# Kernel optimization log

Measured on AMD Instinct MI355X. Metric: run time of the kernel, lower is better.

The kernel has to match this reference:

```python
import jax, jax.numpy as jnp
import numpy as np

WINDOW_SIZE = 5
CONSISTENCY_WEIGHT = 1.0


def _wsum(x, w):
    # sliding-window sum along axis 1 via exclusive cumsum differences
    s = jnp.cumsum(x, axis=1)
    s = jnp.pad(s, ((0, 0), (1, 0)))
    return s[:, w:] - s[:, :-w]  # [B, L-w+1]


def setup_inputs() -> dict:
    key = jax.random.key(0)
    k1, k2, k3 = jax.random.split(key, 3)
    B, L, C = 512, 16384, 2
    return {
        "predictions": jax.random.normal(k1, (B, L, C), dtype=jnp.float32),
        "targets": jax.random.randint(k2, (B, L), 0, 2, dtype=jnp.int32),
        "mask": jax.random.randint(k3, (B, L), 0, 2, dtype=jnp.int32),
    }


def reference(predictions, targets, mask):
    w = WINDOW_SIZE
    probs = jax.nn.softmax(predictions, axis=-1)[..., 1]  # [B, L]
    t = targets.astype(jnp.float32)
    m = mask.astype(jnp.float32)

    msum = _wsum(m, w)                       # [B, W]
    denom = jnp.maximum(msum, 1.0)           # clamp(min=1.0)
    spm = _wsum(probs * m, w)
    stm = _wsum(t * m, w)
    sp2m = _wsum(probs * probs * m, w)
    st2m = _wsum(t * t * m, w)

    pmean = spm / denom
    tmean = stm / denom
    # masked biased variance: sum((x - mean)^2 * m) / clamp(msum, 1)
    pvar = (sp2m - 2.0 * pmean * spm + pmean * pmean * msum) / denom
    tvar = (st2m - 2.0 * tmean * stm + tmean * tmean * msum) / denom

    mse = jnp.mean((pvar - tvar) ** 2, axis=0)          # per-window MSE over batch, [W]
    valid = (jnp.sum(msum, axis=0) > 0).astype(jnp.float32)  # skip windows with zero mask
    cnt = jnp.maximum(jnp.sum(valid), 1.0)
    loss = jnp.sum(mse * valid) / cnt * CONSISTENCY_WEIGHT
    return loss
```

## Files before the change

### kernel.cpp

```cpp
#include <hip/hip_runtime.h>
#include <math.h>

#define BATCH 512
#define LEN   16384
#define WIN   5
#define WOUT  (LEN - WIN + 1)
#define TPB   256
#define TILE  256
#define ELEMS (TILE + WIN - 1)

__global__ void bcl_partial_kernel(const float* __restrict__ pred,
                                   const int*   __restrict__ tgt,
                                   const int*   __restrict__ msk,
                                   float* __restrict__ part_d2,
                                   float* __restrict__ part_ms,
                                   int bper) {
    __shared__ float s_m[ELEMS], s_tm[ELEMS], s_pm[ELEMS], s_p2m[ELEMS];

    const int tile0 = blockIdx.x * TILE;
    const int j     = tile0 + threadIdx.x;
    const int b0    = blockIdx.y * bper;

    float accd2 = 0.f, accms = 0.f;

    for (int b = b0; b < b0 + bper; ++b) {
        __syncthreads();
        for (int i = threadIdx.x; i < ELEMS; i += TPB) {
            const int e = tile0 + i;
            float m = 0.f, tmf = 0.f, p = 0.f;
            if (e < LEN) {
                const size_t base = (size_t)b * LEN + e;
                const int    mi = msk[base];
                const int    ti = tgt[base];
                const float2 p2 = ((const float2*)pred)[base];
                p   = 1.0f / (1.0f + __expf(p2.x - p2.y));
                m   = (float)mi;
                tmf = (float)(ti & mi);
            }
            s_m[i]   = m;
            s_tm[i]  = tmf;
            s_pm[i]  = p * m;
            s_p2m[i] = p * p * m;
        }
        __syncthreads();
        if (j < WOUT) {
            float msum = 0.f, stm = 0.f, spm = 0.f, sp2m = 0.f;
#pragma unroll
            for (int k = 0; k < WIN; ++k) {
                const int i = threadIdx.x + k;
                msum += s_m[i];
                stm  += s_tm[i];
                spm  += s_pm[i];
                sp2m += s_p2m[i];
            }
            const float denom = fmaxf(msum, 1.0f);
            const float inv   = 1.0f / denom;
            const float pmean = spm * inv;
            const float tmean = stm * inv;
            const float pvar  = (sp2m - 2.0f * pmean * spm + pmean * pmean * msum) * inv;
            const float tvar  = (stm  - 2.0f * tmean * stm + tmean * tmean * msum) * inv;
            const float d = pvar - tvar;
            accd2 += d * d;
            accms += msum;
        }
    }
    if (j < WOUT) {
        part_d2[(size_t)blockIdx.y * WOUT + j] = accd2;
        part_ms[(size_t)blockIdx.y * WOUT + j] = accms;
    }
}

__global__ void bcl_window_reduce(const float* __restrict__ part_d2,
                                  const float* __restrict__ part_ms,
                                  double* __restrict__ accum,
                                  unsigned int* __restrict__ ticket,
                                  float* __restrict__ out,
                                  int nchunks) {
    const int j = blockIdx.x * blockDim.x + threadIdx.x;
    double num = 0.0, cnt = 0.0;
    if (j < WOUT) {
        float d2 = 0.f, ms = 0.f;
        for (int c = 0; c < nchunks; ++c) {
            d2 += part_d2[(size_t)c * WOUT + j];
            ms += part_ms[(size_t)c * WOUT + j];
        }
        if (ms > 0.f) {
            num = (double)d2 * (1.0 / (double)BATCH);
            cnt = 1.0;
        }
    }
    for (int off = 32; off > 0; off >>= 1) {
        num += __shfl_down(num, off, 64);
        cnt += __shfl_down(cnt, off, 64);
    }
    __shared__ double s_num[4], s_cnt[4];
    const int lane = threadIdx.x & 63, wave = threadIdx.x >> 6;
    if (lane == 0) { s_num[wave] = num; s_cnt[wave] = cnt; }
    __syncthreads();
    if (threadIdx.x == 0) {
        double n = 0.0, c = 0.0;
        const int nw = (int)(blockDim.x >> 6);
        for (int wv = 0; wv < nw; ++wv) { n += s_num[wv]; c += s_cnt[wv]; }
        atomicAdd(&accum[0], n);
        atomicAdd(&accum[1], c);
        __threadfence();
        const unsigned int t = atomicAdd(ticket, 1u);
        if (t == gridDim.x - 1) {
            out[0] = (float)(accum[0] / fmax(accum[1], 1.0));
        }
    }
}

extern "C" void kernel_launch(void* const* d_in, const int* in_sizes, int n_in,
                              void* d_out, int out_size, void* d_ws, size_t ws_size,
                              hipStream_t stream) {
    const float* pred = (const float*)d_in[0];
    const int*   tgt  = (const int*)d_in[1];
    const int*   msk  = (const int*)d_in[2];
    float* out = (float*)d_out;

    int nchunks = 32;
    while (nchunks > 1) {
        size_t need = (size_t)nchunks * WOUT * 2 * sizeof(float) + 64;
        if (need <= ws_size) break;
        nchunks >>= 1;
    }
    const int bper = BATCH / nchunks;

    float* part_d2 = (float*)d_ws;
    float* part_ms = part_d2 + (size_t)nchunks * WOUT;
    size_t off = ((size_t)nchunks * WOUT * 2 * sizeof(float) + 15) & ~(size_t)15;
    double* accum = (double*)((char*)d_ws + off);
    unsigned int* ticket = (unsigned int*)(accum + 2);

    hipMemsetAsync((void*)accum, 0, 2 * sizeof(double) + sizeof(unsigned int), stream);

    const int WBLKS = (WOUT + TILE - 1) / TILE;

    dim3 g1(WBLKS, nchunks);
    bcl_partial_kernel<<<g1, TPB, 0, stream>>>(pred, tgt, msk, part_d2, part_ms, bper);

    bcl_window_reduce<<<WBLKS, TPB, 0, stream>>>(part_d2, part_ms, accum, ticket, out, nchunks);
}
```

Baseline: 167.9 us.

## Compute sliding windows in registers per thread and reduce partials with atomics

Each thread now owns a run of 16 consecutive windows and loads its 20 input elements with vectorized int4/float4 loads straight into registers. It then updates the window sums incrementally instead of staging tiles in shared memory behind block barriers. Per-chunk partial buffers and the serial chunk loop in the second kernel are replaced by float atomicAdds into a single per-window accumulator, which is zeroed by one memset. This cuts shared-memory traffic and synchronisation and makes the reduce kernel trivial. In exchange it adds strided per-thread loads with poorer coalescing, redundant reads of the 4-element halos, many global atomics, and a nondeterministic summation order.

```diff
diff --git a/kernel.cpp b/kernel.cpp
--- a/kernel.cpp
+++ b/kernel.cpp
@@ -5,85 +5,103 @@
 #define LEN   16384
 #define WIN   5
 #define WOUT  (LEN - WIN + 1)
+#define NW    16
+#define RUNS  ((WOUT + NW - 1) / NW)
+#define NELEM (NW + WIN - 1)
+#define NCHUNK 128
+#define BPER  (BATCH / NCHUNK)
 #define TPB   256
-#define TILE  256
-#define ELEMS (TILE + WIN - 1)
 
-__global__ void bcl_partial_kernel(const float* __restrict__ pred,
-                                   const int*   __restrict__ tgt,
-                                   const int*   __restrict__ msk,
-                                   float* __restrict__ part_d2,
-                                   float* __restrict__ part_ms,
-                                   int bper) {
-    __shared__ float s_m[ELEMS], s_tm[ELEMS], s_pm[ELEMS], s_p2m[ELEMS];
+__device__ __forceinline__ float sigmoid_p(float p0, float p1) {
+    return 1.0f / (1.0f + __expf(p0 - p1));
+}
 
-    const int tile0 = blockIdx.x * TILE;
-    const int j     = tile0 + threadIdx.x;
-    const int b0    = blockIdx.y * bper;
+__global__ void bcl_main_kernel(const float* __restrict__ pred,
+                                const int*   __restrict__ tgt,
+                                const int*   __restrict__ msk,
+                                float* __restrict__ acc_d2,
+                                float* __restrict__ acc_ms) {
+    const int run = blockIdx.x * TPB + threadIdx.x;
+    const int e0  = min(run * NW, LEN - NELEM);
+    const int b0  = blockIdx.y * BPER;
 
-    float accd2 = 0.f, accms = 0.f;
+    float accd2[NW], accms[NW];
+#pragma unroll
+    for (int w = 0; w < NW; ++w) { accd2[w] = 0.f; accms[w] = 0.f; }
 
-    for (int b = b0; b < b0 + bper; ++b) {
-        __syncthreads();
-        for (int i = threadIdx.x; i < ELEMS; i += TPB) {
-            const int e = tile0 + i;
-            float m = 0.f, tmf = 0.f, p = 0.f;
-            if (e < LEN) {
-                const size_t base = (size_t)b * LEN + e;
-                const int    mi = msk[base];
-                const int    ti = tgt[base];
-                const float2 p2 = ((const float2*)pred)[base];
-                p   = 1.0f / (1.0f + __expf(p2.x - p2.y));
-                m   = (float)mi;
-                tmf = (float)(ti & mi);
-            }
-            s_m[i]   = m;
-            s_tm[i]  = tmf;
-            s_pm[i]  = p * m;
-            s_p2m[i] = p * p * m;
+    for (int b = b0; b < b0 + BPER; ++b) {
+        const size_t rowoff = (size_t)b * LEN + e0;
+        const int4*   mv = (const int4*)(msk + rowoff);
+        const int4*   tv = (const int4*)(tgt + rowoff);
+        const float4* pv = (const float4*)(pred + rowoff * 2);
+
+        float m[NELEM], tm[NELEM], pm[NELEM], p2m[NELEM];
+#pragma unroll
+        for (int q = 0; q < NELEM / 4; ++q) {
+            const int4 mm = mv[q];
+            const int4 tt = tv[q];
+            m[4*q+0] = (float)mm.x;  tm[4*q+0] = (float)(tt.x & mm.x);
+            m[4*q+1] = (float)mm.y;  tm[4*q+1] = (float)(tt.y & mm.y);
+            m[4*q+2] = (float)mm.z;  tm[4*q+2] = (float)(tt.z & mm.z);
+            m[4*q+3] = (float)mm.w;  tm[4*q+3] = (float)(tt.w & mm.w);
         }
-        __syncthreads();
-        if (j < WOUT) {
-            float msum = 0.f, stm = 0.f, spm = 0.f, sp2m = 0.f;
 #pragma unroll
-            for (int k = 0; k < WIN; ++k) {
-                const int i = threadIdx.x + k;
-                msum += s_m[i];
-                stm  += s_tm[i];
-                spm  += s_pm[i];
-                sp2m += s_p2m[i];
-            }
-            const float denom = fmaxf(msum, 1.0f);
+        for (int q = 0; q < NELEM / 2; ++q) {
+            const float4 pp = pv[q];
+            const float pa = sigmoid_p(pp.x, pp.y);
+            const float pb = sigmoid_p(pp.z, pp.w);
+            pm [2*q+0] = pa * m[2*q+0];
+            p2m[2*q+0] = pa * pa * m[2*q+0];
+            pm [2*q+1] = pb * m[2*q+1];
+            p2m[2*q+1] = pb * pb * m[2*q+1];
+        }
+
+        float sm  = m[0]  + m[1]  + m[2]  + m[3]  + m[4];
+        float stm = tm[0] + tm[1] + tm[2] + tm[3] + tm[4];
+        float spm = pm[0] + pm[1] + pm[2] + pm[3] + pm[4];
+        float sp2 = p2m[0]+ p2m[1]+ p2m[2]+ p2m[3]+ p2m[4];
+
+#pragma unroll
+        for (int w = 0; w < NW; ++w) {
+            const float denom = fmaxf(sm, 1.0f);
             const float inv   = 1.0f / denom;
             const float pmean = spm * inv;
             const float tmean = stm * inv;
-            const float pvar  = (sp2m - 2.0f * pmean * spm + pmean * pmean * msum) * inv;
-            const float tvar  = (stm  - 2.0f * tmean * stm + tmean * tmean * msum) * inv;
+            const float pvar  = (sp2 - 2.0f * pmean * spm + pmean * pmean * sm) * inv;
+            const float tvar  = (stm - 2.0f * tmean * stm + tmean * tmean * sm) * inv;
             const float d = pvar - tvar;
-            accd2 += d * d;
-            accms += msum;
+            accd2[w] += d * d;
+            accms[w] += sm;
+            if (w < NW - 1) {
+                sm  += m[w + WIN]   - m[w];
+                stm += tm[w + WIN]  - tm[w];
+                spm += pm[w + WIN]  - pm[w];
+                sp2 += p2m[w + WIN] - p2m[w];
+            }
         }
     }
-    if (j < WOUT) {
-        part_d2[(size_t)blockIdx.y * WOUT + j] = accd2;
-        part_ms[(size_t)blockIdx.y * WOUT + j] = accms;
+
+    const int jfirst = run * NW;
+#pragma unroll
+    for (int w = 0; w < NW; ++w) {
+        const int j = e0 + w;
+        if (j >= jfirst) {
+            atomicAdd(&acc_d2[j], accd2[w]);
+            atomicAdd(&acc_ms[j], accms[w]);
+        }
     }
 }
 
-__global__ void bcl_window_reduce(const float* __restrict__ part_d2,
-                                  const float* __restrict__ part_ms,
-                                  double* __restrict__ accum,
-                                  unsigned int* __restrict__ ticket,
-                                  float* __restrict__ out,
-                                  int nchunks) {
+__global__ void bcl_finalize(const float* __restrict__ acc_d2,
+                             const float* __restrict__ acc_ms,
+                             double* __restrict__ accum,
+                             unsigned int* __restrict__ ticket,
+                             float* __restrict__ out) {
     const int j = blockIdx.x * blockDim.x + threadIdx.x;
     double num = 0.0, cnt = 0.0;
     if (j < WOUT) {
-        float d2 = 0.f, ms = 0.f;
-        for (int c = 0; c < nchunks; ++c) {
-            d2 += part_d2[(size_t)c * WOUT + j];
-            ms += part_ms[(size_t)c * WOUT + j];
-        }
+        const float d2 = acc_d2[j];
+        const float ms = acc_ms[j];
         if (ms > 0.f) {
             num = (double)d2 * (1.0 / (double)BATCH);
             cnt = 1.0;
@@ -119,26 +137,18 @@
     const int*   msk  = (const int*)d_in[2];
     float* out = (float*)d_out;
 
-    int nchunks = 32;
-    while (nchunks > 1) {
-        size_t need = (size_t)nchunks * WOUT * 2 * sizeof(float) + 64;
-        if (need <= ws_size) break;
-        nchunks >>= 1;
-    }
-    const int bper = BATCH / nchunks;
-
-    float* part_d2 = (float*)d_ws;
-    float* part_ms = part_d2 + (size_t)nchunks * WOUT;
-    size_t off = ((size_t)nchunks * WOUT * 2 * sizeof(float) + 15) & ~(size_t)15;
+    float* acc_d2 = (float*)d_ws;
+    float* acc_ms = acc_d2 + WOUT;
+    size_t off = ((size_t)WOUT * 2 * sizeof(float) + 15) & ~(size_t)15;
     double* accum = (double*)((char*)d_ws + off);
     unsigned int* ticket = (unsigned int*)(accum + 2);
+    const size_t zbytes = off + 2 * sizeof(double) + sizeof(unsigned int);
 
-    hipMemsetAsync((void*)accum, 0, 2 * sizeof(double) + sizeof(unsigned int), stream);
+    hipMemsetAsync(d_ws, 0, zbytes, stream);
 
-    const int WBLKS = (WOUT + TILE - 1) / TILE;
+    dim3 g1(RUNS / TPB, NCHUNK);
+    bcl_main_kernel<<<g1, TPB, 0, stream>>>(pred, tgt, msk, acc_d2, acc_ms);
 
-    dim3 g1(WBLKS, nchunks);
-    bcl_partial_kernel<<<g1, TPB, 0, stream>>>(pred, tgt, msk, part_d2, part_ms, bper);
-
-    bcl_window_reduce<<<WBLKS, TPB, 0, stream>>>(part_d2, part_ms, accum, ticket, out, nchunks);
+    const int FBLKS = (WOUT + TPB - 1) / TPB;
+    bcl_finalize<<<FBLKS, TPB, 0, stream>>>(acc_d2, acc_ms, accum, ticket, out);
 }
```

New measurement: 399.1 us. 2.38x slower.
